# Performance work log

Hardware: AMD Instinct MI355X
Metric: run time of the kernel (lower is better)

The kernel has to match this reference:

```python
import jax, jax.numpy as jnp
import numpy as np

B = 32768  # batch of intersections (original code is batch=1)
# phase pair construction from the original forward:
# phase_demand[k] = demand[a_k] + demand[b_k]
PAIRS_A = np.array([0, 0, 4, 1, 2, 2, 6, 3])
PAIRS_B = np.array([4, 1, 5, 5, 6, 3, 7, 7])


def _competition_mask():
    m = np.ones((8, 8), np.float32)
    np.fill_diagonal(m, 0.0)
    for i, j in [(0, 1), (0, 2), (1, 3), (2, 3), (4, 5), (4, 6), (5, 7), (6, 7)]:
        m[i, j] = 0.5
        m[j, i] = 0.5
    return jnp.asarray(m)


def setup_inputs() -> dict:
    key = jax.random.key(0)
    ks = jax.random.split(key, 16)
    n = lambda k, shape: jax.random.normal(k, shape, dtype=jnp.float32) * 0.3
    inp = {
        'x': jax.random.normal(ks[0], (B, 16), dtype=jnp.float32),
        'mask': _competition_mask(),
        # demand_model_vehicle: Linear(1,2) ReLU Linear(2,4) ReLU
        'wv1': n(ks[1], (1, 2)), 'bv1': jnp.zeros((2,), jnp.float32),
        'wv2': n(ks[2], (2, 4)), 'bv2': jnp.zeros((4,), jnp.float32),
        # demand_model_phase: Linear(1,2) ReLU Linear(2,4) ReLU
        'wp1': n(ks[3], (1, 2)), 'bp1': jnp.zeros((2,), jnp.float32),
        'wp2': n(ks[4], (2, 4)), 'bp2': jnp.zeros((4,), jnp.float32),
        # embedding: Linear(8,16) ReLU
        'we': n(ks[5], (8, 16)), 'be': jnp.zeros((16,), jnp.float32),
        # conv_pair: 1x1 convs 32->20->20 with ReLU
        'wc1': n(ks[6], (32, 20)), 'bc1': jnp.zeros((20,), jnp.float32),
        'wc2': n(ks[7], (20, 20)), 'bc2': jnp.zeros((20,), jnp.float32),
        # conv_mask_pair: 1x1 convs 1->4->20->20 with ReLU
        'wm1': n(ks[8], (1, 4)), 'bm1': jnp.zeros((4,), jnp.float32),
        'wm2': n(ks[9], (4, 20)), 'bm2': jnp.zeros((20,), jnp.float32),
        'wm3': n(ks[10], (20, 20)), 'bm3': jnp.zeros((20,), jnp.float32),
        # conv_competition: 1x1 convs 20->8->1 (no ReLU)
        'wk1': n(ks[11], (20, 8)), 'bk1': jnp.zeros((8,), jnp.float32),
        'wk2': n(ks[12], (8, 1)), 'bk2': jnp.zeros((1,), jnp.float32),
    }
    return inp


def reference(x, mask, wv1, bv1, wv2, bv2, wp1, bp1, wp2, bp2, we, be,
              wc1, bc1, wc2, bc2, wm1, bm1, wm2, bm2, wm3, bm3,
              wk1, bk1, wk2, bk2):
    b = x.shape[0]
    veh = x[:, :8, None]   # [B,8,1] vehicle counts (fed to demand_model_vehicle)
    pha = x[:, 8:, None]   # [B,8,1] phase bits (fed to demand_model_phase)
    dv = jax.nn.relu(jax.nn.relu(veh @ wv1 + bv1) @ wv2 + bv2)  # [B,8,4]
    dp = jax.nn.relu(jax.nn.relu(pha @ wp1 + bp1) @ wp2 + bp2)  # [B,8,4]
    demand = jax.nn.relu(jnp.concatenate([dv, dp], -1) @ we + be)  # [B,8,16]
    # phase-pair demands
    pd = demand[:, PAIRS_A] + demand[:, PAIRS_B]  # [B,8,16]
    # pairwise concat: pair[i,j] = cat(pd[i], pd[j])  -> [B,8,8,32]
    pair = jnp.concatenate([
        jnp.broadcast_to(pd[:, :, None, :], (b, 8, 8, 16)),
        jnp.broadcast_to(pd[:, None, :, :], (b, 8, 8, 16)),
    ], -1)
    # conv_pair (1x1 convs == channel-dim linears)
    h = jax.nn.relu(pair @ wc1 + bc1)
    h = jax.nn.relu(h @ wc2 + bc2)            # [B,8,8,20]
    # conv_mask_pair on the fixed competition mask
    y = jax.nn.relu(mask[..., None] @ wm1 + bm1)
    y = jax.nn.relu(y @ wm2 + bm2)
    y = jax.nn.relu(y @ wm3 + bm3)            # [8,8,20]
    r = h * y                                  # masked messages [B,8,8,20]
    z = (r @ wk1 + bk1) @ wk2 + bk2            # [B,8,8,1]
    return jnp.sum(z, axis=-1)                 # sum over channel dim -> [B,8,8]
```

## Files before the change

### kernel.cpp

```cpp
#include <hip/hip_runtime.h>

typedef float f32x2 __attribute__((ext_vector_type(2)));
typedef float f32x4 __attribute__((ext_vector_type(4)));

__device__ __forceinline__ float relu_(float v) { return fmaxf(v, 0.f); }
__device__ __forceinline__ void wave_sync() {
    asm volatile("s_waitcnt lgkmcnt(0)" ::: "memory");
}
__device__ __forceinline__ void pk_fma_sw(f32x2& acc, f32x2 hv, f32x2 w) {
    asm("v_pk_fma_f32 %0, %1, %2, %0" : "+v"(acc) : "v"(hv), "s"(w));
}
__device__ __forceinline__ void pk_fma_vv(f32x2& acc, f32x2 a, f32x2 b) {
    asm("v_pk_fma_f32 %0, %1, %2, %0" : "+v"(acc) : "v"(a), "v"(b));
}
__device__ __forceinline__ f32x2 pk_relu(f32x2 a) {
    f32x2 r; r.x = fmaxf(a.x, 0.f); r.y = fmaxf(a.y, 0.f); return r;
}

#define PA_PACK 0x36221400u
#define PB_PACK 0x77365514u

__global__ void yk_kernel(
    const float* __restrict__ mask,
    const float* __restrict__ wm1, const float* __restrict__ bm1,
    const float* __restrict__ wm2, const float* __restrict__ bm2,
    const float* __restrict__ wm3, const float* __restrict__ bm3,
    const float* __restrict__ wk1, const float* __restrict__ bk1,
    const float* __restrict__ wk2, const float* __restrict__ bk2,
    float* __restrict__ ws)
{
    int tid = threadIdx.x;
    int ij = tid >> 2, coff = (tid & 3) * 5;
    int i = ij >> 3, j = ij & 7;
    float m = mask[i * 8 + j];
    float a[4];
#pragma unroll
    for (int q = 0; q < 4; q++) a[q] = relu_(fmaf(m, wm1[q], bm1[q]));
    float b2[20];
#pragma unroll
    for (int c = 0; c < 20; c++) {
        float acc = bm2[c];
#pragma unroll
        for (int q = 0; q < 4; q++) acc = fmaf(a[q], wm2[q * 20 + c], acc);
        b2[c] = relu_(acc);
    }
#pragma unroll
    for (int cc = 0; cc < 5; cc++) {
        int c = coff + cc;
        float acc = bm3[c];
#pragma unroll
        for (int k = 0; k < 20; k++) acc = fmaf(b2[k], wm3[k * 20 + c], acc);
        float y = relu_(acc);
        float wkk = 0.f;
#pragma unroll
        for (int q = 0; q < 8; q++) wkk = fmaf(wk1[c * 8 + q], wk2[q], wkk);
        ws[ij * 20 + c] = y * wkk;
    }
    if (tid == 0) {
        float c0 = bk2[0];
#pragma unroll
        for (int q = 0; q < 8; q++) c0 = fmaf(bk1[q], wk2[q], c0);
        ws[1280] = c0;
    }
}

__global__ __launch_bounds__(256, 5) void frap_kernel(
    const float* __restrict__ x,
    const float* __restrict__ wv1, const float* __restrict__ bv1,
    const float* __restrict__ wv2, const float* __restrict__ bv2,
    const float* __restrict__ wp1, const float* __restrict__ bp1,
    const float* __restrict__ wp2, const float* __restrict__ bp2,
    const float* __restrict__ we,  const float* __restrict__ be,
    const float* __restrict__ wc1, const float* __restrict__ bc1,
    const float* __restrict__ wc2, const float* __restrict__ bc2,
    const float* __restrict__ ykg,
    float* __restrict__ out, int Btot)
{
    __shared__ float s_v[4 * 656];

    const int tid  = threadIdx.x;
    const int w    = tid >> 6;
    const int lane = tid & 63;
    const int g    = lane >> 4;
    const int jh   = (lane >> 3) & 1;
    const int i    = lane & 7;
    const int b    = blockIdx.x * 16 + w * 4 + g;
    const int bb   = (b < Btot) ? b : (Btot - 1);

    const int pa = (PA_PACK >> (4 * i)) & 15;
    const int pb = (PB_PACK >> (4 * i)) & 15;

    float ca[8], cb[8];
    {
        const float xva = x[bb * 16 + pa];
        const float xpa = x[bb * 16 + 8 + pa];
        const float xvb = x[bb * 16 + pb];
        const float xpb = x[bb * 16 + 8 + pb];

        float t0 = relu_(fmaf(xva, wv1[0], bv1[0]));
        float t1 = relu_(fmaf(xva, wv1[1], bv1[1]));
#pragma unroll
        for (int q = 0; q < 4; q++)
            ca[q] = relu_(fmaf(t0, wv2[q], fmaf(t1, wv2[4 + q], bv2[q])));
        float p0 = relu_(fmaf(xpa, wp1[0], bp1[0]));
        float p1 = relu_(fmaf(xpa, wp1[1], bp1[1]));
#pragma unroll
        for (int q = 0; q < 4; q++)
            ca[4 + q] = relu_(fmaf(p0, wp2[q], fmaf(p1, wp2[4 + q], bp2[q])));

        float s0 = relu_(fmaf(xvb, wv1[0], bv1[0]));
        float s1 = relu_(fmaf(xvb, wv1[1], bv1[1]));
#pragma unroll
        for (int q = 0; q < 4; q++)
            cb[q] = relu_(fmaf(s0, wv2[q], fmaf(s1, wv2[4 + q], bv2[q])));
        float r0 = relu_(fmaf(xpb, wp1[0], bp1[0]));
        float r1 = relu_(fmaf(xpb, wp1[1], bp1[1]));
#pragma unroll
        for (int q = 0; q < 4; q++)
            cb[4 + q] = relu_(fmaf(r0, wp2[q], fmaf(r1, wp2[4 + q], bp2[q])));
    }

    float pd[16];
#pragma unroll
    for (int k = 0; k < 16; k++) {
        float da = be[k], db = be[k];
#pragma unroll
        for (int f = 0; f < 8; f++) {
            const float wf = we[f * 16 + k];
            da = fmaf(ca[f], wf, da);
            db = fmaf(cb[f], wf, db);
        }
        pd[k] = relu_(da) + relu_(db);
    }

    f32x2 u2[10];
    union { f32x4 q[5]; f32x2 p[10]; } vvu;
#pragma unroll
    for (int c = 0; c < 10; c++) {
        u2[c] = *(const f32x2*)&bc1[2 * c];
        vvu.p[c].x = 0.f; vvu.p[c].y = 0.f;
    }
#pragma unroll
    for (int k = 0; k < 16; k++) {
        f32x2 pv; pv.x = pd[k]; pv.y = pd[k];
#pragma unroll
        for (int c = 0; c < 10; c++) {
            pk_fma_sw(u2[c],    pv, *(const f32x2*)&wc1[k * 20 + 2 * c]);
            pk_fma_sw(vvu.p[c], pv, *(const f32x2*)&wc1[(16 + k) * 20 + 2 * c]);
        }
    }
    const int vbase = w * 656 + g * 164 + i * 20;
    if (jh == 0) {
#pragma unroll
        for (int p = 0; p < 5; p++)
            *(f32x4*)&s_v[vbase + 4 * p] = vvu.q[p];
    }
    wave_sync();

    const float c0 = ykg[1280];
    const int vg = w * 656 + g * 164;
    const float* __restrict__ ykrow = ykg + i * 160;

#pragma unroll 1
    for (int t = 0; t < 4; t++) {
        const int j = jh * 4 + t;

        union { f32x4 q[5]; float f[20]; } va;
#pragma unroll
        for (int p = 0; p < 5; p++)
            va.q[p] = *(const f32x4*)&s_v[vg + j * 20 + 4 * p];

        f32x2 sA[10];
#pragma unroll
        for (int c = 0; c < 10; c++)
            sA[c] = *(const f32x2*)&bc2[2 * c];
#pragma unroll
        for (int k = 0; k < 20; k++) {
            const float uk = (k & 1) ? u2[k >> 1].y : u2[k >> 1].x;
            const float hA = relu_(uk + va.f[k]);
            f32x2 hva; hva.x = hA; hva.y = hA;
#pragma unroll
            for (int c = 0; c < 10; c++)
                pk_fma_sw(sA[c], hva, *(const f32x2*)&wc2[k * 20 + 2 * c]);
        }

        union { f32x4 q[5]; f32x2 p[10]; } ya;
#pragma unroll
        for (int p = 0; p < 5; p++)
            ya.q[p] = *(const f32x4*)&ykrow[j * 20 + 4 * p];
        f32x2 z2; z2.x = 0.f; z2.y = 0.f;
#pragma unroll
        for (int c = 0; c < 10; c++)
            pk_fma_vv(z2, pk_relu(sA[c]), ya.p[c]);
        if (b < Btot)
            out[b * 64 + i * 8 + j] = c0 + z2.x + z2.y;
    }
}

extern "C" void kernel_launch(void* const* d_in, const int* in_sizes, int n_in,
                              void* d_out, int out_size, void* d_ws, size_t ws_size,
                              hipStream_t stream) {
    const float* x    = (const float*)d_in[0];
    const float* mask = (const float*)d_in[1];
    const float* wv1  = (const float*)d_in[2];
    const float* bv1  = (const float*)d_in[3];
    const float* wv2  = (const float*)d_in[4];
    const float* bv2  = (const float*)d_in[5];
    const float* wp1  = (const float*)d_in[6];
    const float* bp1  = (const float*)d_in[7];
    const float* wp2  = (const float*)d_in[8];
    const float* bp2  = (const float*)d_in[9];
    const float* we   = (const float*)d_in[10];
    const float* be   = (const float*)d_in[11];
    const float* wc1  = (const float*)d_in[12];
    const float* bc1  = (const float*)d_in[13];
    const float* wc2  = (const float*)d_in[14];
    const float* bc2  = (const float*)d_in[15];
    const float* wm1  = (const float*)d_in[16];
    const float* bm1  = (const float*)d_in[17];
    const float* wm2  = (const float*)d_in[18];
    const float* bm2  = (const float*)d_in[19];
    const float* wm3  = (const float*)d_in[20];
    const float* bm3  = (const float*)d_in[21];
    const float* wk1  = (const float*)d_in[22];
    const float* bk1  = (const float*)d_in[23];
    const float* wk2  = (const float*)d_in[24];
    const float* bk2  = (const float*)d_in[25];
    float* out = (float*)d_out;
    float* ws  = (float*)d_ws;

    int Btot = in_sizes[0] / 16;

    yk_kernel<<<1, 256, 0, stream>>>(mask, wm1, bm1, wm2, bm2, wm3, bm3,
                                     wk1, bk1, wk2, bk2, ws);

    int grid = (Btot + 15) / 16;
    frap_kernel<<<grid, 256, 0, stream>>>(
        x, wv1, bv1, wv2, bv2, wp1, bp1, wp2, bp2, we, be,
        wc1, bc1, wc2, bc2, ws, out, Btot);
}
```

Baseline: 42.84 us.

## Split conv_pair work across lane halves and stage U/V halves through LDS

Each lane now computes only one half of the first conv_pair projection: jh=0 lanes compute the U term with bias, jh=1 lanes compute the V term. Both are written to a larger shared buffer instead of U staying in registers. The second conv is processed in two 10-channel halves. The yk workspace is repadded to 24-float rows and the launch_bounds hint is removed. The goal is to cut register pressure and redundant FMA work, at the cost of more LDS traffic and a shared-memory footprint that grows from about 10 KB to 20 KB.

Result: slower. 63.38 us (+48.0%).

```diff
diff --git a/kernel.cpp b/kernel.cpp
--- a/kernel.cpp
+++ b/kernel.cpp
@@ -9,12 +9,6 @@
 }
 __device__ __forceinline__ void pk_fma_sw(f32x2& acc, f32x2 hv, f32x2 w) {
     asm("v_pk_fma_f32 %0, %1, %2, %0" : "+v"(acc) : "v"(hv), "s"(w));
-}
-__device__ __forceinline__ void pk_fma_vv(f32x2& acc, f32x2 a, f32x2 b) {
-    asm("v_pk_fma_f32 %0, %1, %2, %0" : "+v"(acc) : "v"(a), "v"(b));
-}
-__device__ __forceinline__ f32x2 pk_relu(f32x2 a) {
-    f32x2 r; r.x = fmaxf(a.x, 0.f); r.y = fmaxf(a.y, 0.f); return r;
 }
 
 #define PA_PACK 0x36221400u
@@ -54,17 +48,18 @@
         float wkk = 0.f;
 #pragma unroll
         for (int q = 0; q < 8; q++) wkk = fmaf(wk1[c * 8 + q], wk2[q], wkk);
-        ws[ij * 20 + c] = y * wkk;
+        int half = (c >= 10), cc12 = c - 10 * half;
+        ws[ij * 24 + half * 12 + cc12] = y * wkk;
     }
     if (tid == 0) {
         float c0 = bk2[0];
 #pragma unroll
         for (int q = 0; q < 8; q++) c0 = fmaf(bk1[q], wk2[q], c0);
-        ws[1280] = c0;
-    }
-}
-
-__global__ __launch_bounds__(256, 5) void frap_kernel(
+        ws[1536] = c0;
+    }
+}
+
+__global__ void frap_kernel(
     const float* __restrict__ x,
     const float* __restrict__ wv1, const float* __restrict__ bv1,
     const float* __restrict__ wv2, const float* __restrict__ bv2,
@@ -76,7 +71,7 @@
     const float* __restrict__ ykg,
     float* __restrict__ out, int Btot)
 {
-    __shared__ float s_v[4 * 656];
+    __shared__ float s_uv[16 * 16 * 20];
 
     const int tid  = threadIdx.x;
     const int w    = tid >> 6;
@@ -133,67 +128,81 @@
         pd[k] = relu_(da) + relu_(db);
     }
 
-    f32x2 u2[10];
-    union { f32x4 q[5]; f32x2 p[10]; } vvu;
-#pragma unroll
-    for (int c = 0; c < 10; c++) {
-        u2[c] = *(const f32x2*)&bc1[2 * c];
-        vvu.p[c].x = 0.f; vvu.p[c].y = 0.f;
-    }
-#pragma unroll
-    for (int k = 0; k < 16; k++) {
-        f32x2 pv; pv.x = pd[k]; pv.y = pd[k];
-#pragma unroll
-        for (int c = 0; c < 10; c++) {
-            pk_fma_sw(u2[c],    pv, *(const f32x2*)&wc1[k * 20 + 2 * c]);
-            pk_fma_sw(vvu.p[c], pv, *(const f32x2*)&wc1[(16 + k) * 20 + 2 * c]);
-        }
-    }
-    const int vbase = w * 656 + g * 164 + i * 20;
-    if (jh == 0) {
-#pragma unroll
-        for (int p = 0; p < 5; p++)
-            *(f32x4*)&s_v[vbase + 4 * p] = vvu.q[p];
+    const int myrow = ((w * 4 + g) * 16 + jh * 8 + i) * 20;
+    const int wrow  = jh * 16;
+#pragma unroll
+    for (int half = 0; half < 2; half++) {
+        f32x2 acc[5];
+#pragma unroll
+        for (int c = 0; c < 5; c++) {
+            if (jh == 0) acc[c] = *(const f32x2*)&bc1[half * 10 + 2 * c];
+            else { acc[c].x = 0.f; acc[c].y = 0.f; }
+        }
+#pragma unroll
+        for (int k = 0; k < 16; k++) {
+            f32x2 pv; pv.x = pd[k]; pv.y = pd[k];
+#pragma unroll
+            for (int c = 0; c < 5; c++)
+                pk_fma_sw(acc[c], pv,
+                          *(const f32x2*)&wc1[(wrow + k) * 20 + half * 10 + 2 * c]);
+        }
+#pragma unroll
+        for (int c = 0; c < 5; c++)
+            *(f32x2*)&s_uv[myrow + half * 10 + 2 * c] = acc[c];
     }
     wave_sync();
 
-    const float c0 = ykg[1280];
-    const int vg = w * 656 + g * 164;
-    const float* __restrict__ ykrow = ykg + i * 160;
+    const float c0 = ykg[1536];
+    const int gbase = (w * 4 + g) * 16 * 20;
+    const float* __restrict__ ykrow = ykg + i * 192;
 
 #pragma unroll 1
     for (int t = 0; t < 4; t++) {
         const int j = jh * 4 + t;
 
-        union { f32x4 q[5]; float f[20]; } va;
-#pragma unroll
-        for (int p = 0; p < 5; p++)
-            va.q[p] = *(const f32x4*)&s_v[vg + j * 20 + 4 * p];
-
-        f32x2 sA[10];
-#pragma unroll
-        for (int c = 0; c < 10; c++)
-            sA[c] = *(const f32x2*)&bc2[2 * c];
-#pragma unroll
-        for (int k = 0; k < 20; k++) {
-            const float uk = (k & 1) ? u2[k >> 1].y : u2[k >> 1].x;
-            const float hA = relu_(uk + va.f[k]);
-            f32x2 hva; hva.x = hA; hva.y = hA;
-#pragma unroll
-            for (int c = 0; c < 10; c++)
-                pk_fma_sw(sA[c], hva, *(const f32x2*)&wc2[k * 20 + 2 * c]);
-        }
-
-        union { f32x4 q[5]; f32x2 p[10]; } ya;
-#pragma unroll
-        for (int p = 0; p < 5; p++)
-            ya.q[p] = *(const f32x4*)&ykrow[j * 20 + 4 * p];
-        f32x2 z2; z2.x = 0.f; z2.y = 0.f;
-#pragma unroll
-        for (int c = 0; c < 10; c++)
-            pk_fma_vv(z2, pk_relu(sA[c]), ya.p[c]);
+        float h1[20];
+#pragma unroll
+        for (int p = 0; p < 5; p++) {
+            f32x4 uq = *(const f32x4*)&s_uv[gbase + i * 20 + 4 * p];
+            f32x4 vq = *(const f32x4*)&s_uv[gbase + (8 + j) * 20 + 4 * p];
+            h1[4*p+0] = relu_(uq.x + vq.x);
+            h1[4*p+1] = relu_(uq.y + vq.y);
+            h1[4*p+2] = relu_(uq.z + vq.z);
+            h1[4*p+3] = relu_(uq.w + vq.w);
+        }
+
+        float z = 0.f;
+#pragma unroll
+        for (int half = 0; half < 2; half++) {
+            f32x2 sA[5];
+#pragma unroll
+            for (int c = 0; c < 5; c++)
+                sA[c] = *(const f32x2*)&bc2[half * 10 + 2 * c];
+#pragma unroll
+            for (int k = 0; k < 20; k++) {
+                f32x2 hv; hv.x = h1[k]; hv.y = h1[k];
+#pragma unroll
+                for (int c = 0; c < 5; c++)
+                    pk_fma_sw(sA[c], hv,
+                              *(const f32x2*)&wc2[k * 20 + half * 10 + 2 * c]);
+            }
+            const float* yh = ykrow + j * 24 + half * 12;
+            f32x4 y0 = *(const f32x4*)&yh[0];
+            f32x4 y1 = *(const f32x4*)&yh[4];
+            f32x2 y2 = *(const f32x2*)&yh[8];
+            z = fmaf(relu_(sA[0].x), y0.x, z);
+            z = fmaf(relu_(sA[0].y), y0.y, z);
+            z = fmaf(relu_(sA[1].x), y0.z, z);
+            z = fmaf(relu_(sA[1].y), y0.w, z);
+            z = fmaf(relu_(sA[2].x), y1.x, z);
+            z = fmaf(relu_(sA[2].y), y1.y, z);
+            z = fmaf(relu_(sA[3].x), y1.z, z);
+            z = fmaf(relu_(sA[3].y), y1.w, z);
+            z = fmaf(relu_(sA[4].x), y2.x, z);
+            z = fmaf(relu_(sA[4].y), y2.y, z);
+        }
         if (b < Btot)
-            out[b * 64 + i * 8 + j] = c0 + z2.x + z2.y;
+            out[b * 64 + i * 8 + j] = c0 + z;
     }
 }
 
```
